# Kernel optimization log

Hardware: AMD Instinct MI355X
Metric: run time of the kernel (lower is better)

The kernel has to match this reference:

```python
import jax, jax.numpy as jnp
import numpy as np

B, D, C = 4096, 4096, 1024


def setup_inputs() -> dict:
    key = jax.random.key(0)
    kx, kw = jax.random.split(key)
    x = jax.random.normal(kx, (B, D), dtype=jnp.float32)
    # kaiming_normal_ with nonlinearity='relu': std = sqrt(2 / fan_in)
    W = jax.random.normal(kw, (C, D), dtype=jnp.float32) * jnp.sqrt(2.0 / D)
    return {"x": x, "W": W}


def reference(x, W):
    # Original: -( (x[:, :, None] - W.T[None, :, :])**2 ).mean(axis=1)
    d = x.shape[1]
    x_sq = jnp.sum(x * x, axis=1, keepdims=True)        # [B, 1]
    w_sq = jnp.sum(W * W, axis=1)[None, :]              # [1, C]
    cross = jnp.einsum('bd,cd->bc', x, W)               # [B, C] tensor-core GEMM
    return -(x_sq - 2.0 * cross + w_sq) / d
```

## Files before the change

### kernel.cpp

```cpp
#include <hip/hip_runtime.h>
#include <hip/hip_bf16.h>


typedef float f32x4 __attribute__((ext_vector_type(4)));
typedef unsigned short ushort4_t __attribute__((ext_vector_type(4)));

#define BDIM 4096
#define DDIM 4096
#define CDIM 1024
#define TM 128
#define TN 128
#define BK 64
#define KSPLIT 4
#define SCALE 32.0f
#define INV_SS (1.0f/1024.0f)

__device__ __forceinline__ unsigned short f2bf(float f) {
    unsigned int u = __float_as_uint(f);
    unsigned int rounding = 0x7FFFu + ((u >> 16) & 1u);
    return (unsigned short)((u + rounding) >> 16);
}

__global__ __launch_bounds__(256) void cvt_rowsq(
    const float* __restrict__ x, const float* __restrict__ W,
    unsigned char* __restrict__ xb, unsigned char* __restrict__ wb,
    float* __restrict__ xsq, float* __restrict__ wsq)
{
    const int lane = threadIdx.x & 63;
    const int row = blockIdx.x * 4 + (threadIdx.x >> 6);

    const float* src;
    unsigned char* dst;
    float* sq;
    if (row < BDIM) {
        src = x + (size_t)row * DDIM;
        dst = xb + (size_t)row * DDIM;
        sq = xsq + row;
    } else {
        int r = row - BDIM;
        src = W + (size_t)r * DDIM;
        dst = wb + (size_t)r * DDIM;
        sq = wsq + r;
    }

    const float4* s4 = (const float4*)src;
    unsigned int* d4 = (unsigned int*)dst;
    float a = 0.f;
    #pragma unroll
    for (int s = 0; s < DDIM / 4 / 64; ++s) {
        float4 f = s4[lane + 64 * s];
        a += f.x * f.x + f.y * f.y + f.z * f.z + f.w * f.w;
        unsigned int p = 0;
        p = __builtin_amdgcn_cvt_pk_fp8_f32(f.x * SCALE, f.y * SCALE, p, false);
        p = __builtin_amdgcn_cvt_pk_fp8_f32(f.z * SCALE, f.w * SCALE, p, true);
        d4[lane + 64 * s] = p;
    }
    #pragma unroll
    for (int off = 32; off > 0; off >>= 1) a += __shfl_down(a, off);
    if (lane == 0) *sq = a;
}

__global__ __launch_bounds__(256, 4) void gemm_eucl(
    const unsigned char* __restrict__ xb,
    const unsigned char* __restrict__ wb,
    unsigned short* __restrict__ part)
{
    __shared__ unsigned char As[TM * BK];
    __shared__ unsigned char Bs[TN * BK];

    const int tid = threadIdx.x;
    const int lane = tid & 63;
    const int wid = tid >> 6;
    const int bm = blockIdx.x * TM;
    const int bn = blockIdx.y * TN;
    const int ks = blockIdx.z * (DDIM / KSPLIT);
    const int wm = (wid >> 1) * 64;
    const int wn = (wid & 1) * 64;

    const int r0 = tid >> 2, s0 = tid & 3;
    const int g0 = s0 ^ (r0 & 3);
    const int r1 = (tid + 256) >> 2, s1 = tid & 3;
    const int g1 = s1 ^ (r1 & 3);
    const unsigned char* gA0 = xb + (size_t)(bm + r0) * DDIM + ks + g0 * 16;
    const unsigned char* gA1 = xb + (size_t)(bm + r1) * DDIM + ks + g1 * 16;
    const unsigned char* gB0 = wb + (size_t)(bn + r0) * DDIM + ks + g0 * 16;
    const unsigned char* gB1 = wb + (size_t)(bn + r1) * DDIM + ks + g1 * 16;

    const int kc = lane >> 4;
    const int ml = lane & 15;
    int aoff[4][2], boff[4][2];
    #pragma unroll
    for (int i = 0; i < 4; ++i) {
        #pragma unroll
        for (int k2 = 0; k2 < 2; ++k2) {
            int c = (k2 * 32 + kc * 8) >> 4;
            int bo = (kc & 1) * 8;
            int m = wm + i * 16 + ml;
            aoff[i][k2] = m * BK + ((c ^ (m & 3)) * 16) + bo;
            int n = wn + i * 16 + ml;
            boff[i][k2] = n * BK + ((c ^ (n & 3)) * 16) + bo;
        }
    }

    f32x4 acc[4][4] = {};

    for (int k0 = 0; k0 < DDIM / KSPLIT; k0 += BK) {
        __syncthreads();
        __builtin_amdgcn_global_load_lds(
            (__attribute__((address_space(1))) const void*)gA0,
            (__attribute__((address_space(3))) void*)(&As[tid * 16]), 16, 0, 0);
        __builtin_amdgcn_global_load_lds(
            (__attribute__((address_space(1))) const void*)gA1,
            (__attribute__((address_space(3))) void*)(&As[tid * 16 + 4096]), 16, 0, 0);
        __builtin_amdgcn_global_load_lds(
            (__attribute__((address_space(1))) const void*)gB0,
            (__attribute__((address_space(3))) void*)(&Bs[tid * 16]), 16, 0, 0);
        __builtin_amdgcn_global_load_lds(
            (__attribute__((address_space(1))) const void*)gB1,
            (__attribute__((address_space(3))) void*)(&Bs[tid * 16 + 4096]), 16, 0, 0);
        gA0 += BK; gA1 += BK; gB0 += BK; gB1 += BK;
        __syncthreads();

        long af[4][2], bf[4][2];
        #pragma unroll
        for (int i = 0; i < 4; ++i) {
            af[i][0] = *(const long*)&As[aoff[i][0]];
            af[i][1] = *(const long*)&As[aoff[i][1]];
        }
        #pragma unroll
        for (int j = 0; j < 4; ++j) {
            bf[j][0] = *(const long*)&Bs[boff[j][0]];
            bf[j][1] = *(const long*)&Bs[boff[j][1]];
        }
        #pragma unroll
        for (int i = 0; i < 4; ++i)
            #pragma unroll
            for (int j = 0; j < 4; ++j) {
                acc[i][j] = __builtin_amdgcn_mfma_f32_16x16x32_fp8_fp8(
                    af[i][0], bf[j][0], acc[i][j], 0, 0, 0);
                acc[i][j] = __builtin_amdgcn_mfma_f32_16x16x32_fp8_fp8(
                    af[i][1], bf[j][1], acc[i][j], 0, 0, 0);
            }
    }

    unsigned short* p = part + (size_t)blockIdx.z * BDIM * CDIM
                      + (size_t)(blockIdx.x * 8 + blockIdx.y) * 16384;
    #pragma unroll
    for (int i = 0; i < 4; ++i)
        #pragma unroll
        for (int j = 0; j < 4; ++j) {
            ushort4_t v;
            v[0] = f2bf(acc[i][j][0]); v[1] = f2bf(acc[i][j][1]);
            v[2] = f2bf(acc[i][j][2]); v[3] = f2bf(acc[i][j][3]);
            *(ushort4_t*)&p[(i * 4 + j) * 1024 + tid * 4] = v;
        }
}

__global__ __launch_bounds__(256) void reduce_out(
    const unsigned short* __restrict__ part, const float* __restrict__ xsq,
    const float* __restrict__ wsq, float* __restrict__ out)
{
    const int bb = blockIdx.x;
    const int t = threadIdx.x;
    const int lane = t & 63;
    const int wid = t >> 6;
    const int bm = (bb >> 3) * TM, bn = (bb & 7) * TN;
    const int wm = (wid >> 1) * 64, wn = (wid & 1) * 64;
    const int row_l = (lane >> 4) * 4, col_l = lane & 15;
    const size_t sl = (size_t)BDIM * CDIM;
    const float c1 = 2.0f * INV_SS / (float)DDIM;
    const float c2 = 1.0f / (float)DDIM;

    #pragma unroll
    for (int f = 0; f < 16; ++f) {
        size_t o = (size_t)bb * 16384 + f * 1024 + t * 4;
        ushort4_t p0 = *(const ushort4_t*)&part[o];
        ushort4_t p1 = *(const ushort4_t*)&part[o + sl];
        ushort4_t p2 = *(const ushort4_t*)&part[o + 2 * sl];
        ushort4_t p3 = *(const ushort4_t*)&part[o + 3 * sl];
        int i = f >> 2, j = f & 3;
        int gn = bn + wn + j * 16 + col_l;
        float wv = wsq[gn];
        #pragma unroll
        for (int r = 0; r < 4; ++r) {
            float s = __uint_as_float((unsigned int)p0[r] << 16)
                    + __uint_as_float((unsigned int)p1[r] << 16)
                    + __uint_as_float((unsigned int)p2[r] << 16)
                    + __uint_as_float((unsigned int)p3[r] << 16);
            int gm = bm + wm + i * 16 + row_l + r;
            out[(size_t)gm * CDIM + gn] = s * c1 - (xsq[gm] + wv) * c2;
        }
    }
}

__global__ void fallback_kernel(const float* __restrict__ x, const float* __restrict__ W,
                                float* __restrict__ out)
{
    int c = blockIdx.x * blockDim.x + threadIdx.x;
    int b = blockIdx.y;
    if (c >= CDIM) return;
    const float* xr = x + (size_t)b * DDIM;
    const float* wr = W + (size_t)c * DDIM;
    float xs = 0.f, ws = 0.f, cr = 0.f;
    for (int d = 0; d < DDIM; ++d) {
        float xv = xr[d], wv = wr[d];
        xs += xv * xv; ws += wv * wv; cr += xv * wv;
    }
    out[(size_t)b * CDIM + c] = (2.0f * cr - xs - ws) / (float)DDIM;
}

extern "C" void kernel_launch(void* const* d_in, const int* in_sizes, int n_in,
                              void* d_out, int out_size, void* d_ws, size_t ws_size,
                              hipStream_t stream) {
    const float* x = (const float*)d_in[0];
    const float* W = (const float*)d_in[1];
    float* out = (float*)d_out;

    size_t need = (size_t)(BDIM + CDIM) * DDIM
                + (size_t)(BDIM + CDIM) * sizeof(float)
                + (size_t)KSPLIT * BDIM * CDIM * 2;
    if (ws_size < need) {
        fallback_kernel<<<dim3(CDIM / 256, BDIM), 256, 0, stream>>>(x, W, out);
        return;
    }

    unsigned char* xb = (unsigned char*)d_ws;
    unsigned char* wb = xb + (size_t)BDIM * DDIM;
    float* xsq = (float*)(wb + (size_t)CDIM * DDIM);
    float* wsq = xsq + BDIM;
    unsigned short* part = (unsigned short*)(wsq + CDIM);

    cvt_rowsq<<<(BDIM + CDIM) / 4, 256, 0, stream>>>(x, W, xb, wb, xsq, wsq);
    gemm_eucl<<<dim3(BDIM / TM, CDIM / TN, KSPLIT), 256, 0, stream>>>(xb, wb, part);
    reduce_out<<<256, 256, 0, stream>>>(part, xsq, wsq, out);
}
```

Before: 156.4 us.

## Double-buffer LDS with register-staged prefetch and k-permuted layout in fp8 GEMM

Replaces the direct global-to-LDS loads with register prefetch of the next K tile into a second LDS buffer while MFMAs consume the current one, leaving one barrier per iteration instead of two. The LDS layout is permuted along K so each lane fetches both MFMA operands with a single 16-byte LDS read instead of two 8-byte reads. The cost is doubled shared memory, higher register pressure, occupancy lowered to 3 blocks per SIMD, and explicit LDS store instructions.

After: 149.9 us. -4.2%, faster.

```diff
diff --git a/kernel.cpp b/kernel.cpp
--- a/kernel.cpp
+++ b/kernel.cpp
@@ -4,6 +4,7 @@
 
 typedef float f32x4 __attribute__((ext_vector_type(4)));
 typedef unsigned short ushort4_t __attribute__((ext_vector_type(4)));
+typedef long long2_t __attribute__((ext_vector_type(2)));
 
 #define BDIM 4096
 #define DDIM 4096
@@ -12,6 +13,7 @@
 #define TN 128
 #define BK 64
 #define KSPLIT 4
+#define NIT ((DDIM / KSPLIT) / BK)
 #define SCALE 32.0f
 #define INV_SS (1.0f/1024.0f)
 
@@ -60,13 +62,12 @@
     if (lane == 0) *sq = a;
 }
 
-__global__ __launch_bounds__(256, 4) void gemm_eucl(
+__global__ __launch_bounds__(256, 3) void gemm_eucl(
     const unsigned char* __restrict__ xb,
     const unsigned char* __restrict__ wb,
     unsigned short* __restrict__ part)
 {
-    __shared__ unsigned char As[TM * BK];
-    __shared__ unsigned char Bs[TN * BK];
+    __shared__ unsigned char sm[2 * 16384];
 
     const int tid = threadIdx.x;
     const int lane = tid & 63;
@@ -77,69 +78,97 @@
     const int wm = (wid >> 1) * 64;
     const int wn = (wid & 1) * 64;
 
-    const int r0 = tid >> 2, s0 = tid & 3;
-    const int g0 = s0 ^ (r0 & 3);
-    const int r1 = (tid + 256) >> 2, s1 = tid & 3;
-    const int g1 = s1 ^ (r1 & 3);
-    const unsigned char* gA0 = xb + (size_t)(bm + r0) * DDIM + ks + g0 * 16;
-    const unsigned char* gA1 = xb + (size_t)(bm + r1) * DDIM + ks + g1 * 16;
-    const unsigned char* gB0 = wb + (size_t)(bn + r0) * DDIM + ks + g0 * 16;
-    const unsigned char* gB1 = wb + (size_t)(bn + r1) * DDIM + ks + g1 * 16;
+    const int r0 = tid >> 2, c = tid & 3;
+    const unsigned char* gA0 = xb + (size_t)(bm + r0) * DDIM + ks + c * 16;
+    const unsigned char* gA1 = gA0 + (size_t)64 * DDIM;
+    const unsigned char* gB0 = wb + (size_t)(bn + r0) * DDIM + ks + c * 16;
+    const unsigned char* gB1 = gB0 + (size_t)64 * DDIM;
+
+    const int k2o = (c >> 1) * 8;
+    const int kcw = (c & 1) * 2;
+    const int wo0 = r0 * 64 + ((kcw ^ (r0 & 3)) * 16) + k2o;
+    const int wo1 = r0 * 64 + (((kcw | 1) ^ (r0 & 3)) * 16) + k2o;
 
     const int kc = lane >> 4;
     const int ml = lane & 15;
-    int aoff[4][2], boff[4][2];
+    int aoff[4], boff[4];
     #pragma unroll
     for (int i = 0; i < 4; ++i) {
-        #pragma unroll
-        for (int k2 = 0; k2 < 2; ++k2) {
-            int c = (k2 * 32 + kc * 8) >> 4;
-            int bo = (kc & 1) * 8;
-            int m = wm + i * 16 + ml;
-            aoff[i][k2] = m * BK + ((c ^ (m & 3)) * 16) + bo;
-            int n = wn + i * 16 + ml;
-            boff[i][k2] = n * BK + ((c ^ (n & 3)) * 16) + bo;
-        }
+        int m = wm + i * 16 + ml;
+        aoff[i] = m * 64 + ((kc ^ (m & 3)) * 16);
+        int n = wn + i * 16 + ml;
+        boff[i] = n * 64 + ((kc ^ (n & 3)) * 16);
     }
 
     f32x4 acc[4][4] = {};
-
-    for (int k0 = 0; k0 < DDIM / KSPLIT; k0 += BK) {
+    long2_t pA0, pA1, pB0, pB1;
+
+    pA0 = *(const long2_t*)gA0; pA1 = *(const long2_t*)gA1;
+    pB0 = *(const long2_t*)gB0; pB1 = *(const long2_t*)gB1;
+    gA0 += BK; gA1 += BK; gB0 += BK; gB1 += BK;
+    {
+        unsigned char* sA = sm;
+        unsigned char* sB = sm + 8192;
+        *(long*)(sA + wo0) = pA0.x; *(long*)(sA + wo1) = pA0.y;
+        *(long*)(sA + wo0 + 4096) = pA1.x; *(long*)(sA + wo1 + 4096) = pA1.y;
+        *(long*)(sB + wo0) = pB0.x; *(long*)(sB + wo1) = pB0.y;
+        *(long*)(sB + wo0 + 4096) = pB1.x; *(long*)(sB + wo1 + 4096) = pB1.y;
+    }
+    __syncthreads();
+
+    int pb = 0;
+    for (int k = 0; k < NIT - 1; ++k) {
+        pA0 = *(const long2_t*)gA0; pA1 = *(const long2_t*)gA1;
+        pB0 = *(const long2_t*)gB0; pB1 = *(const long2_t*)gB1;
+        gA0 += BK; gA1 += BK; gB0 += BK; gB1 += BK;
+
+        {
+            const unsigned char* sA = sm + pb * 16384;
+            const unsigned char* sB = sA + 8192;
+            long2_t la[4], lb[4];
+            #pragma unroll
+            for (int i = 0; i < 4; ++i) la[i] = *(const long2_t*)(sA + aoff[i]);
+            #pragma unroll
+            for (int j = 0; j < 4; ++j) lb[j] = *(const long2_t*)(sB + boff[j]);
+            #pragma unroll
+            for (int i = 0; i < 4; ++i)
+                #pragma unroll
+                for (int j = 0; j < 4; ++j) {
+                    acc[i][j] = __builtin_amdgcn_mfma_f32_16x16x32_fp8_fp8(
+                        la[i].x, lb[j].x, acc[i][j], 0, 0, 0);
+                    acc[i][j] = __builtin_amdgcn_mfma_f32_16x16x32_fp8_fp8(
+                        la[i].y, lb[j].y, acc[i][j], 0, 0, 0);
+                }
+        }
+
+        {
+            unsigned char* sA = sm + (pb ^ 1) * 16384;
+            unsigned char* sB = sA + 8192;
+            *(long*)(sA + wo0) = pA0.x; *(long*)(sA + wo1) = pA0.y;
+            *(long*)(sA + wo0 + 4096) = pA1.x; *(long*)(sA + wo1 + 4096) = pA1.y;
+            *(long*)(sB + wo0) = pB0.x; *(long*)(sB + wo1) = pB0.y;
+            *(long*)(sB + wo0 + 4096) = pB1.x; *(long*)(sB + wo1 + 4096) = pB1.y;
+        }
         __syncthreads();
-        __builtin_amdgcn_global_load_lds(
-            (__attribute__((address_space(1))) const void*)gA0,
-            (__attribute__((address_space(3))) void*)(&As[tid * 16]), 16, 0, 0);
-        __builtin_amdgcn_global_load_lds(
-            (__attribute__((address_space(1))) const void*)gA1,
-            (__attribute__((address_space(3))) void*)(&As[tid * 16 + 4096]), 16, 0, 0);
-        __builtin_amdgcn_global_load_lds(
-            (__attribute__((address_space(1))) const void*)gB0,
-            (__attribute__((address_space(3))) void*)(&Bs[tid * 16]), 16, 0, 0);
-        __builtin_amdgcn_global_load_lds(
-            (__attribute__((address_space(1))) const void*)gB1,
-            (__attribute__((address_space(3))) void*)(&Bs[tid * 16 + 4096]), 16, 0, 0);
-        gA0 += BK; gA1 += BK; gB0 += BK; gB1 += BK;
-        __syncthreads();
-
-        long af[4][2], bf[4][2];
-        #pragma unroll
-        for (int i = 0; i < 4; ++i) {
-            af[i][0] = *(const long*)&As[aoff[i][0]];
-            af[i][1] = *(const long*)&As[aoff[i][1]];
-        }
-        #pragma unroll
-        for (int j = 0; j < 4; ++j) {
-            bf[j][0] = *(const long*)&Bs[boff[j][0]];
-            bf[j][1] = *(const long*)&Bs[boff[j][1]];
-        }
+        pb ^= 1;
+    }
+
+    {
+        const unsigned char* sA = sm + pb * 16384;
+        const unsigned char* sB = sA + 8192;
+        long2_t la[4], lb[4];
+        #pragma unroll
+        for (int i = 0; i < 4; ++i) la[i] = *(const long2_t*)(sA + aoff[i]);
+        #pragma unroll
+        for (int j = 0; j < 4; ++j) lb[j] = *(const long2_t*)(sB + boff[j]);
         #pragma unroll
         for (int i = 0; i < 4; ++i)
             #pragma unroll
             for (int j = 0; j < 4; ++j) {
                 acc[i][j] = __builtin_amdgcn_mfma_f32_16x16x32_fp8_fp8(
-                    af[i][0], bf[j][0], acc[i][j], 0, 0, 0);
+                    la[i].x, lb[j].x, acc[i][j], 0, 0, 0);
                 acc[i][j] = __builtin_amdgcn_mfma_f32_16x16x32_fp8_fp8(
-                    af[i][1], bf[j][1], acc[i][j], 0, 0, 0);
+                    la[i].y, lb[j].y, acc[i][j], 0, 0, 0);
             }
     }
 
```
